# Kernel optimization log

Hardware: AMD Instinct MI355X
Metric: run time of the kernel (lower is better)

The kernel has to match this reference:

```python
import jax, jax.numpy as jnp
import numpy as np

START = 5.0
STEP = 8
SIZE = 256
STOP = SIZE // 2 - 1.0  # self.stop = int(size/2) - 1.0
# Original loops over tf.linspace(s, stop, step) and truncates each value to int.
US = [int(v) for v in np.linspace(START, STOP, STEP)]


def _block_mask(w, h, u):
    # Boolean block of ones of size (2u+1)^2 centered at (w//2, h//2).
    # Original: dd[half_w-u:half_w+u+1, half_h-u:half_h+u+1] = 1, then keeps
    # only that region of the shifted spectrum (ideal low-pass filter).
    m = np.zeros((w, h), dtype=np.float32)
    m[w // 2 - u: w // 2 + u + 1, h // 2 - u: h // 2 + u + 1] = 1.0
    return jnp.asarray(m)


def setup_inputs() -> dict:
    key = jax.random.key(0)
    x = jax.random.normal(key, (64, SIZE, SIZE, 1), dtype=jnp.float32)
    return {"x": x}


def reference(x):
    n, w, h, c = x.shape  # c == 1
    im = x[..., 0].astype(jnp.complex64)  # [n, w, h]
    # FFT is identical across loop iterations in the original; hoist it.
    # fftshift/ifftshift over all axes in TF cancel on the batch axis, so
    # shifting only the spatial axes is mathematically identical.
    freq = jnp.fft.fftshift(jnp.fft.fft2(im), axes=(-2, -1))
    outs = [x]
    for u in US:  # small fixed loop over STEP cutoff radii
        mask = _block_mask(w, h, u)
        low = freq * mask.astype(jnp.complex64)  # keep low frequencies only
        out = jnp.real(jnp.fft.ifft2(jnp.fft.ifftshift(low, axes=(-2, -1))))
        outs.append(out.astype(x.dtype)[..., None])
    return jnp.concatenate(outs, axis=-1)  # [n, w, h, STEP+1]
```

## Files before the change

### kernel.cpp

```cpp
#include <hip/hip_runtime.h>

typedef __attribute__((ext_vector_type(4))) float          f32x4;
typedef __attribute__((ext_vector_type(2))) float          f32x2;
typedef __attribute__((ext_vector_type(4))) unsigned int   u32x4;
typedef __attribute__((ext_vector_type(4))) unsigned short u16x4;
typedef __attribute__((ext_vector_type(2))) unsigned short u16x2;

#define PI_F 3.14159265358979f

__device__ __forceinline__ unsigned short f2bf(float f) {
    unsigned int x = __float_as_uint(f);
    unsigned int r = ((x >> 16) & 1u) + 0x7fffu;
    return (unsigned short)((x + r) >> 16);
}
__device__ __forceinline__ float bf2f(unsigned short v) {
    return __uint_as_float((unsigned int)v << 16);
}
__device__ __forceinline__ void mfma16(f32x4& c, u32x4 a, u32x4 b) {
    asm volatile("v_mfma_f32_16x16x32_bf16 %0, %1, %2, %0"
                 : "+v"(c) : "v"(a), "v"(b));
}


__global__ void prep(const float* __restrict__ x, unsigned short* __restrict__ H,
                     unsigned short* __restrict__ Xb, float* __restrict__ out,
                     int write_c0) {
    int b = blockIdx.x;
    if (b < 2048) {
        const int US[8] = {5, 22, 39, 57, 74, 92, 109, 127};
        int idx = b * 256 + threadIdx.x;
        int u = idx >> 16;
        int i = (idx >> 8) & 255, js = idx & 255;
        int jl = js ^ ((i & 7) << 3);
        int d = (i - jl) & 255;
        int m = 2 * US[u] + 1;
        float h;
        if (d == 0) {
            h = (float)m * (1.0f / 256.0f);
        } else {
            int t = (m * d) & 511;
            float num = sinf((float)t * (PI_F / 256.0f));
            float den = sinf((float)d * (PI_F / 256.0f));
            h = num / (256.0f * den);
        }
        H[idx] = f2bf(h);
    } else {
        int idx = (b - 2048) * 256 + threadIdx.x;
        f32x4 v = ((const f32x4*)x)[idx];
        u16x4 o = { f2bf(v.x), f2bf(v.y), f2bf(v.z), f2bf(v.w) };
        int n = idx >> 14;
        int t = idx & 16383;
        int i = t >> 6;
        int jlin = (t & 63) * 4;
        int js = jlin ^ ((i & 7) << 3);
        *(u16x4*)(Xb + (size_t)n * 65536 + i * 256 + js) = o;
        if (write_c0) {
            size_t g = (size_t)idx * 4;
            out[(g + 0) * 9] = v.x;
            out[(g + 1) * 9] = v.y;
            out[(g + 2) * 9] = v.z;
            out[(g + 3) * 9] = v.w;
        }
    }
}

__global__ void __launch_bounds__(256) stage12(const unsigned short* __restrict__ Xb,
                                               const unsigned short* __restrict__ H,
                                               unsigned short* __restrict__ Zb,
                                               float* __restrict__ fOut,
                                               int mode, int u_fixed) {
    __shared__ char sT[32768];

    int n, u, jq;
    if (u_fixed >= 0) {
        n = blockIdx.x >> 2; jq = blockIdx.x & 3; u = u_fixed;
    } else {
        int swz = (blockIdx.x & 7) * 256 + (blockIdx.x >> 3);
        n = swz >> 5; u = (swz >> 2) & 7; jq = swz & 3;
    }

    const char* Xn = (const char*)(Xb + (size_t)n * 65536);
    const char* Hu = (const char*)(H + (size_t)u * 65536);

    const int tid  = threadIdx.x;
    const int lane = tid & 63;
    const int w    = tid >> 6;
    const int lrow = lane & 15;
    const int lk   = lane >> 4;
    const int lmask = (lrow & 7) << 4;
    const int offk0 = (lk * 16) ^ lmask;
    const int offk1 = (64 + lk * 16) ^ lmask;

    f32x4 acc[4][4];
#pragma unroll
    for (int a = 0; a < 4; ++a)
#pragma unroll
        for (int b = 0; b < 4; ++b) acc[a][b] = (f32x4){0.f, 0.f, 0.f, 0.f};

#pragma unroll
    for (int kt = 0; kt < 4; ++kt) {
#pragma unroll
        for (int kk = 0; kk < 2; ++kk) {
            const int off = kt * 128 + (kk ? offk1 : offk0);
            u32x4 af[4], bf[4];
#pragma unroll
            for (int mi = 0; mi < 4; ++mi)
                af[mi] = *(const u32x4*)(Xn + (w * 64 + mi * 16 + lrow) * 512 + off);
#pragma unroll
            for (int ni = 0; ni < 4; ++ni)
                bf[ni] = *(const u32x4*)(Hu + (jq * 64 + ni * 16 + lrow) * 512 + off);
#pragma unroll
            for (int mi = 0; mi < 4; ++mi)
#pragma unroll
                for (int ni = 0; ni < 4; ++ni)
                    mfma16(acc[mi][ni], af[mi], bf[ni]);
        }
    }
    asm volatile("s_nop 7\n\ts_nop 7");

#pragma unroll
    for (int mi = 0; mi < 4; ++mi) {
        int i4 = w * 64 + mi * 16 + (lane >> 4) * 4;
#pragma unroll
        for (int ni = 0; ni < 4; ++ni) {
            int jl = ni * 16 + lrow;
            u16x4 o = { f2bf(acc[mi][ni].x), f2bf(acc[mi][ni].y),
                        f2bf(acc[mi][ni].z), f2bf(acc[mi][ni].w) };
            *(u16x4*)(sT + jl * 512 + ((2 * i4) ^ ((jl & 7) << 4))) = o;
        }
    }
    __syncthreads();

#pragma unroll
    for (int a = 0; a < 4; ++a)
#pragma unroll
        for (int b = 0; b < 4; ++b) acc[a][b] = (f32x4){0.f, 0.f, 0.f, 0.f};

#pragma unroll
    for (int kt = 0; kt < 4; ++kt) {
#pragma unroll
        for (int kk = 0; kk < 2; ++kk) {
            const int off = kt * 128 + (kk ? offk1 : offk0);
            u32x4 af[4], bf[4];
#pragma unroll
            for (int mi = 0; mi < 4; ++mi)
                af[mi] = *(const u32x4*)(sT + (mi * 16 + lrow) * 512 + off);
#pragma unroll
            for (int ni = 0; ni < 4; ++ni)
                bf[ni] = *(const u32x4*)(Hu + (w * 64 + ni * 16 + lrow) * 512 + off);
#pragma unroll
            for (int mi = 0; mi < 4; ++mi)
#pragma unroll
                for (int ni = 0; ni < 4; ++ni)
                    mfma16(acc[mi][ni], af[mi], bf[ni]);
        }
    }
    asm volatile("s_nop 7\n\ts_nop 7");

    if (mode == 0) {
        unsigned short* Op = Zb + ((size_t)(u * 64 + n)) * 65536 + jq * 64;
#pragma unroll
        for (int mi = 0; mi < 4; ++mi) {
            int r4 = mi * 16 + (lane >> 4) * 4;
#pragma unroll
            for (int ni = 0; ni < 4; ++ni) {
                int c = w * 64 + ni * 16 + lrow;
                u16x4 o = { f2bf(acc[mi][ni].x), f2bf(acc[mi][ni].y),
                            f2bf(acc[mi][ni].z), f2bf(acc[mi][ni].w) };
                *(u16x4*)(Op + (size_t)c * 256 + r4) = o;
            }
        }
    } else {
#pragma unroll
        for (int mi = 0; mi < 4; ++mi) {
            int r4 = mi * 16 + (lane >> 4) * 4;
#pragma unroll
            for (int ni = 0; ni < 4; ++ni) {
                int c = w * 64 + ni * 16 + lrow;
                float* o = fOut + (((size_t)n * 256 + c) * 256 + jq * 64 + r4) * 9 + 1 + u;
                o[0]  = acc[mi][ni].x;
                o[9]  = acc[mi][ni].y;
                o[18] = acc[mi][ni].z;
                o[27] = acc[mi][ni].w;
            }
        }
    }
}

__global__ void __launch_bounds__(256) pack9(const float* __restrict__ x,
                                             const unsigned short* __restrict__ Zb,
                                             float* __restrict__ out) {
    __shared__ float sl[9216];
    const int t = threadIdx.x;
    const size_t g0 = (size_t)blockIdx.x * 1024;

#pragma unroll
    for (int c = 0; c < 2; ++c) {
        int q = c * 512 + t * 2;
        size_t p = g0 + q;
        f32x2 xv = *(const f32x2*)(x + p);
        sl[q * 9]       = xv.x;
        sl[(q + 1) * 9] = xv.y;
#pragma unroll
        for (int u = 0; u < 8; ++u) {
            u16x2 z = *(const u16x2*)(Zb + (size_t)u * 4194304 + p);
            sl[q * 9 + 1 + u]       = bf2f(z.x);
            sl[(q + 1) * 9 + 1 + u] = bf2f(z.y);
        }
    }
    __syncthreads();
    float* ob = out + g0 * 9;
#pragma unroll
    for (int r = 0; r < 9; ++r) {
        int d = r * 1024 + t * 4;
        *(f32x4*)(ob + d) = *(const f32x4*)&sl[d];
    }
}

extern "C" void kernel_launch(void* const* d_in, const int* in_sizes, int n_in,
                              void* d_out, int out_size, void* d_ws, size_t ws_size,
                              hipStream_t stream) {
    const float* x = (const float*)d_in[0];
    float* out = (float*)d_out;
    char* ws = (char*)d_ws;

    unsigned short* H  = (unsigned short*)(ws);
    unsigned short* Xb = (unsigned short*)(ws + 1048576);
    unsigned short* Zb = (unsigned short*)(ws + 9437184);

    const size_t NEED_FULL = 76546048ull;

    if (ws_size >= NEED_FULL) {
        prep<<<6144, 256, 0, stream>>>(x, H, Xb, out, 0);
        stage12<<<2048, 256, 0, stream>>>(Xb, H, Zb, nullptr, 0, -1);
        pack9<<<4096, 256, 0, stream>>>(x, Zb, out);
    } else {
        prep<<<6144, 256, 0, stream>>>(x, H, Xb, out, 1);
        for (int u = 0; u < 8; ++u)
            stage12<<<256, 256, 0, stream>>>(Xb, H, nullptr, out, 1, u);
    }
}
```

Measured before the change: 104.3 us.

## Stage per-wave GEMM operands through LDS with direct global-to-LDS loads

Both GEMM phases in stage12 now stage the per-wave operand tiles (X rows in phase one, H rows in phase two) into a private LDS buffer using global_load_lds 16-byte loads, then read the MFMA fragments from LDS instead of issuing strided 16-byte global loads per lane. Explicit waitcnt fences and sched barriers order the transfers, and s_setprio raises wave priority around the MFMA bursts. The intent is more coalesced global traffic and fewer VGPR-routed loads. In exchange, LDS use doubles to 64 KB per block, which can reduce occupancy, and the full vmcnt(0) waits serialize load and compute within each k-tile.

```diff
diff --git a/kernel.cpp b/kernel.cpp
--- a/kernel.cpp
+++ b/kernel.cpp
@@ -6,6 +6,9 @@
 typedef __attribute__((ext_vector_type(4))) unsigned short u16x4;
 typedef __attribute__((ext_vector_type(2))) unsigned short u16x2;
 
+typedef const unsigned int __attribute__((address_space(1)))* gas_ptr;
+typedef unsigned int __attribute__((address_space(3)))*       las_ptr;
+
 #define PI_F 3.14159265358979f
 
 __device__ __forceinline__ unsigned short f2bf(float f) {
@@ -19,6 +22,18 @@
 __device__ __forceinline__ void mfma16(f32x4& c, u32x4 a, u32x4 b) {
     asm volatile("v_mfma_f32_16x16x32_bf16 %0, %1, %2, %0"
                  : "+v"(c) : "v"(a), "v"(b));
+}
+__device__ __forceinline__ void gload16(const void* g, void* l) {
+    __builtin_amdgcn_global_load_lds((gas_ptr)g, (las_ptr)l, 16, 0, 0);
+}
+__device__ __forceinline__ void fence_lgkm0() {
+    asm volatile("s_waitcnt lgkmcnt(0)" ::: "memory");
+    __builtin_amdgcn_sched_barrier(0);
+}
+__device__ __forceinline__ void fence_vm0() {
+    __builtin_amdgcn_sched_barrier(0);
+    asm volatile("s_waitcnt vmcnt(0)" ::: "memory");
+    __builtin_amdgcn_sched_barrier(0);
 }
 
 
@@ -69,6 +84,7 @@
                                                unsigned short* __restrict__ Zb,
                                                float* __restrict__ fOut,
                                                int mode, int u_fixed) {
+    __shared__ char sStage[32768];
     __shared__ char sT[32768];
 
     int n, u, jq;
@@ -90,6 +106,8 @@
     const int lmask = (lrow & 7) << 4;
     const int offk0 = (lk * 16) ^ lmask;
     const int offk1 = (64 + lk * 16) ^ lmask;
+    const int srow = lane >> 3, sch = lane & 7;
+    char* myS = sStage + w * 8192;
 
     f32x4 acc[4][4];
 #pragma unroll
@@ -97,23 +115,33 @@
 #pragma unroll
         for (int b = 0; b < 4; ++b) acc[a][b] = (f32x4){0.f, 0.f, 0.f, 0.f};
 
-#pragma unroll
     for (int kt = 0; kt < 4; ++kt) {
+        fence_lgkm0();
+#pragma unroll
+        for (int q = 0; q < 8; ++q) {
+            int r = (w * 8 + q) * 8 + srow;
+            gload16(Xn + r * 512 + kt * 128 + sch * 16, myS + q * 1024);
+        }
 #pragma unroll
         for (int kk = 0; kk < 2; ++kk) {
-            const int off = kt * 128 + (kk ? offk1 : offk0);
-            u32x4 af[4], bf[4];
-#pragma unroll
-            for (int mi = 0; mi < 4; ++mi)
-                af[mi] = *(const u32x4*)(Xn + (w * 64 + mi * 16 + lrow) * 512 + off);
+            const int off  = kt * 128 + (kk ? offk1 : offk0);
+            const int loff = kk ? offk1 : offk0;
+            u32x4 bf[4];
 #pragma unroll
             for (int ni = 0; ni < 4; ++ni)
                 bf[ni] = *(const u32x4*)(Hu + (jq * 64 + ni * 16 + lrow) * 512 + off);
+            if (kk == 0) fence_vm0();
+            u32x4 af[4];
+#pragma unroll
+            for (int mi = 0; mi < 4; ++mi)
+                af[mi] = *(const u32x4*)(myS + (mi * 16 + lrow) * 128 + loff);
+            __builtin_amdgcn_s_setprio(1);
 #pragma unroll
             for (int mi = 0; mi < 4; ++mi)
 #pragma unroll
                 for (int ni = 0; ni < 4; ++ni)
                     mfma16(acc[mi][ni], af[mi], bf[ni]);
+            __builtin_amdgcn_s_setprio(0);
         }
     }
     asm volatile("s_nop 7\n\ts_nop 7");
@@ -136,23 +164,32 @@
 #pragma unroll
         for (int b = 0; b < 4; ++b) acc[a][b] = (f32x4){0.f, 0.f, 0.f, 0.f};
 
-#pragma unroll
     for (int kt = 0; kt < 4; ++kt) {
+        fence_lgkm0();
+#pragma unroll
+        for (int q = 0; q < 8; ++q) {
+            int r = (w * 8 + q) * 8 + srow;
+            gload16(Hu + r * 512 + kt * 128 + sch * 16, myS + q * 1024);
+        }
+        fence_vm0();
 #pragma unroll
         for (int kk = 0; kk < 2; ++kk) {
-            const int off = kt * 128 + (kk ? offk1 : offk0);
+            const int off  = kt * 128 + (kk ? offk1 : offk0);
+            const int loff = kk ? offk1 : offk0;
             u32x4 af[4], bf[4];
 #pragma unroll
             for (int mi = 0; mi < 4; ++mi)
                 af[mi] = *(const u32x4*)(sT + (mi * 16 + lrow) * 512 + off);
 #pragma unroll
             for (int ni = 0; ni < 4; ++ni)
-                bf[ni] = *(const u32x4*)(Hu + (w * 64 + ni * 16 + lrow) * 512 + off);
+                bf[ni] = *(const u32x4*)(myS + (ni * 16 + lrow) * 128 + loff);
+            __builtin_amdgcn_s_setprio(1);
 #pragma unroll
             for (int mi = 0; mi < 4; ++mi)
 #pragma unroll
                 for (int ni = 0; ni < 4; ++ni)
                     mfma16(acc[mi][ni], af[mi], bf[ni]);
+            __builtin_amdgcn_s_setprio(0);
         }
     }
     asm volatile("s_nop 7\n\ts_nop 7");
```

Result: faster. 98.88 us (-5.2%).

## Stage H tile in LDS via async loads and double-buffer global operand loads

Applied to the files above, without the earlier changes.

The shared H tile used in the first GEMM is now copied into LDS with global_load_lds, so all four waves read it from LDS instead of each fetching it from global memory. Global operand fragments for both GEMMs are software-pipelined with two register buffers, so the loads for the next k-tile are issued before the current tile's MFMAs. Launch bounds now request two blocks per SM. This raises LDS use to 64KB per block and adds register pressure, which may limit occupancy.

```diff
diff --git a/kernel.cpp b/kernel.cpp
--- a/kernel.cpp
+++ b/kernel.cpp
@@ -6,6 +6,9 @@
 typedef __attribute__((ext_vector_type(4))) unsigned short u16x4;
 typedef __attribute__((ext_vector_type(2))) unsigned short u16x2;
 
+typedef const unsigned int __attribute__((address_space(1)))* gas_ptr;
+typedef unsigned int __attribute__((address_space(3)))*       las_ptr;
+
 #define PI_F 3.14159265358979f
 
 __device__ __forceinline__ unsigned short f2bf(float f) {
@@ -19,6 +22,9 @@
 __device__ __forceinline__ void mfma16(f32x4& c, u32x4 a, u32x4 b) {
     asm volatile("v_mfma_f32_16x16x32_bf16 %0, %1, %2, %0"
                  : "+v"(c) : "v"(a), "v"(b));
+}
+__device__ __forceinline__ void gload16(const void* g, void* l) {
+    __builtin_amdgcn_global_load_lds((gas_ptr)g, (las_ptr)l, 16, 0, 0);
 }
 
 
@@ -64,11 +70,44 @@
     }
 }
 
-__global__ void __launch_bounds__(256) stage12(const unsigned short* __restrict__ Xb,
-                                               const unsigned short* __restrict__ H,
-                                               unsigned short* __restrict__ Zb,
-                                               float* __restrict__ fOut,
-                                               int mode, int u_fixed) {
+#define LOAD_A(dst, KT)                                                        \
+    _Pragma("unroll") for (int kk = 0; kk < 2; ++kk)                           \
+    _Pragma("unroll") for (int mi = 0; mi < 4; ++mi)                           \
+        dst[kk * 4 + mi] = *(const u32x4*)(Arow[mi] + (KT) * 128 + offA[kk]);
+
+#define COMPUTE_A(BUF, KT)                                                     \
+    _Pragma("unroll") for (int kk = 0; kk < 2; ++kk) {                         \
+        u32x4 bf[4];                                                           \
+        _Pragma("unroll") for (int ni = 0; ni < 4; ++ni)                       \
+            bf[ni] = *(const u32x4*)(sHq + (ni * 16 + lrow) * 512 +            \
+                                     (KT) * 128 + offA[kk]);                   \
+        _Pragma("unroll") for (int mi = 0; mi < 4; ++mi)                       \
+        _Pragma("unroll") for (int ni = 0; ni < 4; ++ni)                       \
+            mfma16(acc[mi][ni], BUF[kk * 4 + mi], bf[ni]);                     \
+    }
+
+#define LOAD_B(dst, KT)                                                        \
+    _Pragma("unroll") for (int kk = 0; kk < 2; ++kk)                           \
+    _Pragma("unroll") for (int ni = 0; ni < 4; ++ni)                           \
+        dst[kk * 4 + ni] = *(const u32x4*)(Brow[ni] + (KT) * 128 + offA[kk]);
+
+#define COMPUTE_B(BUF, KT)                                                     \
+    _Pragma("unroll") for (int kk = 0; kk < 2; ++kk) {                         \
+        u32x4 af[4];                                                           \
+        _Pragma("unroll") for (int mi = 0; mi < 4; ++mi)                       \
+            af[mi] = *(const u32x4*)(sT + (mi * 16 + lrow) * 512 +             \
+                                     (KT) * 128 + offA[kk]);                   \
+        _Pragma("unroll") for (int mi = 0; mi < 4; ++mi)                       \
+        _Pragma("unroll") for (int ni = 0; ni < 4; ++ni)                       \
+            mfma16(acc[mi][ni], af[mi], BUF[kk * 4 + ni]);                     \
+    }
+
+__global__ void __launch_bounds__(256, 2) stage12(const unsigned short* __restrict__ Xb,
+                                                  const unsigned short* __restrict__ H,
+                                                  unsigned short* __restrict__ Zb,
+                                                  float* __restrict__ fOut,
+                                                  int mode, int u_fixed) {
+    __shared__ char sHq[32768];
     __shared__ char sT[32768];
 
     int n, u, jq;
@@ -88,8 +127,23 @@
     const int lrow = lane & 15;
     const int lk   = lane >> 4;
     const int lmask = (lrow & 7) << 4;
-    const int offk0 = (lk * 16) ^ lmask;
-    const int offk1 = (64 + lk * 16) ^ lmask;
+    const int offA[2] = { (lk * 16) ^ lmask, (64 + lk * 16) ^ lmask };
+
+#pragma unroll
+    for (int q = 0; q < 8; ++q)
+        gload16(Hu + jq * 32768 + (w * 8 + q) * 1024 + lane * 16,
+                sHq + (w * 8 + q) * 1024);
+
+    const char* Arow[4];
+#pragma unroll
+    for (int mi = 0; mi < 4; ++mi)
+        Arow[mi] = Xn + (w * 64 + mi * 16 + lrow) * 512;
+
+    u32x4 aC[8], aN[8];
+    LOAD_A(aC, 0)
+    LOAD_A(aN, 1)
+
+    __syncthreads();
 
     f32x4 acc[4][4];
 #pragma unroll
@@ -97,25 +151,12 @@
 #pragma unroll
         for (int b = 0; b < 4; ++b) acc[a][b] = (f32x4){0.f, 0.f, 0.f, 0.f};
 
-#pragma unroll
-    for (int kt = 0; kt < 4; ++kt) {
-#pragma unroll
-        for (int kk = 0; kk < 2; ++kk) {
-            const int off = kt * 128 + (kk ? offk1 : offk0);
-            u32x4 af[4], bf[4];
-#pragma unroll
-            for (int mi = 0; mi < 4; ++mi)
-                af[mi] = *(const u32x4*)(Xn + (w * 64 + mi * 16 + lrow) * 512 + off);
-#pragma unroll
-            for (int ni = 0; ni < 4; ++ni)
-                bf[ni] = *(const u32x4*)(Hu + (jq * 64 + ni * 16 + lrow) * 512 + off);
-#pragma unroll
-            for (int mi = 0; mi < 4; ++mi)
-#pragma unroll
-                for (int ni = 0; ni < 4; ++ni)
-                    mfma16(acc[mi][ni], af[mi], bf[ni]);
-        }
-    }
+    COMPUTE_A(aC, 0)
+    LOAD_A(aC, 2)
+    COMPUTE_A(aN, 1)
+    LOAD_A(aN, 3)
+    COMPUTE_A(aC, 2)
+    COMPUTE_A(aN, 3)
     asm volatile("s_nop 7\n\ts_nop 7");
 
 #pragma unroll
@@ -136,25 +177,19 @@
 #pragma unroll
         for (int b = 0; b < 4; ++b) acc[a][b] = (f32x4){0.f, 0.f, 0.f, 0.f};
 
-#pragma unroll
-    for (int kt = 0; kt < 4; ++kt) {
-#pragma unroll
-        for (int kk = 0; kk < 2; ++kk) {
-            const int off = kt * 128 + (kk ? offk1 : offk0);
-            u32x4 af[4], bf[4];
-#pragma unroll
-            for (int mi = 0; mi < 4; ++mi)
-                af[mi] = *(const u32x4*)(sT + (mi * 16 + lrow) * 512 + off);
-#pragma unroll
-            for (int ni = 0; ni < 4; ++ni)
-                bf[ni] = *(const u32x4*)(Hu + (w * 64 + ni * 16 + lrow) * 512 + off);
-#pragma unroll
-            for (int mi = 0; mi < 4; ++mi)
-#pragma unroll
-                for (int ni = 0; ni < 4; ++ni)
-                    mfma16(acc[mi][ni], af[mi], bf[ni]);
-        }
-    }
+    const char* Brow[4];
+#pragma unroll
+    for (int ni = 0; ni < 4; ++ni)
+        Brow[ni] = Hu + (w * 64 + ni * 16 + lrow) * 512;
+
+    LOAD_B(aC, 0)
+    LOAD_B(aN, 1)
+    COMPUTE_B(aC, 0)
+    LOAD_B(aC, 2)
+    COMPUTE_B(aN, 1)
+    LOAD_B(aN, 3)
+    COMPUTE_B(aC, 2)
+    COMPUTE_B(aN, 3)
     asm volatile("s_nop 7\n\ts_nop 7");
 
     if (mode == 0) {
```

Result: faster. 93.44 us (-10.4%).
